# Kernel optimization log

Hardware: AMD Instinct MI355X
Metric: run time of the kernel (lower is better)

## Reference

```python
import jax, jax.numpy as jnp
import numpy as np

N0, N1, N2 = 20000, 15000, 15000
N = N0 + N1 + N2          # total nodes
E = 800000                # edges
H, D = 4, 64              # heads, hidden per head
ED = 64                   # edge feature dim
NET = 8                   # num edge types
C = 16                    # num classes
SLOPE = 0.2               # leaky relu negative slope
ALPHA = 0.05              # residual-attention mixing

def _glorot(key, shape):
    return jax.random.normal(key, shape, dtype=jnp.float32) / jnp.sqrt(jnp.float32(shape[-1]))

def setup_inputs() -> dict:
    key = jax.random.key(0)
    ks = jax.random.split(key, 32)
    return {
        "x0": jax.random.normal(ks[0], (N0, 128), jnp.float32),
        "x1": jax.random.normal(ks[1], (N1, 64), jnp.float32),
        "x2": jax.random.normal(ks[2], (N2, 32), jnp.float32),
        "src": jax.random.randint(ks[3], (E,), 0, N),
        "dst": jax.random.randint(ks[4], (E,), 0, N),
        "efeat": jax.random.randint(ks[5], (E,), 0, NET),
        # per-node-type input projections (fc_list)
        "W0": _glorot(ks[6], (64, 128)), "b0": jnp.zeros((64,), jnp.float32),
        "W1": _glorot(ks[7], (64, 64)),  "b1": jnp.zeros((64,), jnp.float32),
        "W2": _glorot(ks[8], (64, 32)),  "b2": jnp.zeros((64,), jnp.float32),
        # GAT layer 0: in 64 -> H*D, no residual, elu
        "Wg0": _glorot(ks[9], (H * D, 64)),
        "etab0": _glorot(ks[10], (NET, ED)),
        "We0": _glorot(ks[11], (H * ED, ED)),
        "al0": _glorot(ks[12], (H, D)), "ar0": _glorot(ks[13], (H, D)), "ae0": _glorot(ks[14], (H, ED)),
        # GAT layer 1: in H*D -> H*D, identity residual, elu
        "Wg1": _glorot(ks[15], (H * D, H * D)),
        "etab1": _glorot(ks[16], (NET, ED)),
        "We1": _glorot(ks[17], (H * ED, ED)),
        "al1": _glorot(ks[18], (H, D)), "ar1": _glorot(ks[19], (H, D)), "ae1": _glorot(ks[20], (H, ED)),
        # final GAT layer: in H*D -> 1*C, linear residual, no activation
        "Wg2": _glorot(ks[21], (C, H * D)),
        "etab2": _glorot(ks[22], (NET, ED)),
        "We2": _glorot(ks[23], (ED, ED)),
        "al2": _glorot(ks[24], (1, C)), "ar2": _glorot(ks[25], (1, C)), "ae2": _glorot(ks[26], (1, ED)),
        "resW2": _glorot(ks[27], (C, H * D)),
    }

def _edge_softmax(scores, dst):
    # softmax over incoming edges of each dst node; scores: [E, H]
    m = jax.ops.segment_max(scores, dst, num_segments=N)
    ex = jnp.exp(scores - m[dst])
    s = jax.ops.segment_sum(ex, dst, num_segments=N)
    return ex / (s[dst] + 1e-9)

def _gat_conv(h, src, dst, et, Wg, etab, We, al, ar, ae, res_attn, res, resW, act):
    nH, oD = al.shape
    feat = (h @ Wg.T).reshape(N, nH, oD)                 # [N,H,D]
    ee = (etab[et] @ We.T).reshape(E, nH, -1)            # [E,H,ED]
    el = jnp.einsum('nhd,hd->nh', feat, al)
    er = jnp.einsum('nhd,hd->nh', feat, ar)
    es = jnp.einsum('ehd,hd->eh', ee, ae)
    logits = jax.nn.leaky_relu(el[src] + er[dst] + es, SLOPE)
    a = _edge_softmax(logits, dst)                       # [E,H]
    if res_attn is not None:
        a = a * (1.0 - ALPHA) + res_attn * ALPHA
    out = jax.ops.segment_sum(a[:, :, None] * feat[src], dst, num_segments=N)
    if res:
        resval = (h @ resW.T).reshape(N, -1, oD) if resW is not None else h.reshape(N, nH, oD)
        out = out + resval
    if act is not None:
        out = act(out)
    return out, jax.lax.stop_gradient(a)                 # attention detached (res_attn)

def reference(x0, x1, x2, src, dst, efeat, W0, b0, W1, b1, W2, b2,
              Wg0, etab0, We0, al0, ar0, ae0,
              Wg1, etab1, We1, al1, ar1, ae1,
              Wg2, etab2, We2, al2, ar2, ae2, resW2):
    h = jnp.concatenate([x0 @ W0.T + b0, x1 @ W1.T + b1, x2 @ W2.T + b2], axis=0)  # [N,64]
    h, ra = _gat_conv(h, src, dst, efeat, Wg0, etab0, We0, al0, ar0, ae0, None, False, None, jax.nn.elu)
    h = h.reshape(N, -1)
    h, ra = _gat_conv(h, src, dst, efeat, Wg1, etab1, We1, al1, ar1, ae1, ra, True, None, jax.nn.elu)
    h = h.reshape(N, -1)
    logits, _ = _gat_conv(h, src, dst, efeat, Wg2, etab2, We2, al2, ar2, ae2, None, True, resW2, None)
    return logits.mean(axis=1)                           # [N, C]
```

## Files before the change

### kernel.cpp

```cpp
#include <hip/hip_runtime.h>
#include <math.h>

#define N0 20000
#define N1 15000
#define N2 15000
#define NN 50000
#define EE 800000
#define SLOPE 0.2f
#define ALPHA 0.05f

typedef _Float16 h8 __attribute__((ext_vector_type(8)));
typedef _Float16 h4 __attribute__((ext_vector_type(4)));
typedef float f4v __attribute__((ext_vector_type(4)));

__device__ __forceinline__ float sel4(float4 v, int h) {
    float lo = (h & 1) ? v.y : v.x;
    float hi = (h & 1) ? v.w : v.z;
    return (h & 2) ? hi : lo;
}

__device__ __forceinline__ float elu_fast(float x) {
    return x > 0.f ? x : __expf(x) - 1.f;
}


__global__ void hist_kernel(const int* __restrict__ dst, int* __restrict__ deg, int E_) {
    int e = blockIdx.x * blockDim.x + threadIdx.x;
    if (e < E_) atomicAdd(&deg[dst[e]], 1);
}

__global__ __launch_bounds__(256) void block_sum_kernel(const int* __restrict__ deg,
                                                        int* __restrict__ bsum, int n) {
    int i = blockIdx.x * 256 + threadIdx.x;
    int v = (i < n) ? deg[i] : 0;
    #pragma unroll
    for (int off = 32; off > 0; off >>= 1) v += __shfl_down(v, off);
    __shared__ int sh[4];
    if ((threadIdx.x & 63) == 0) sh[threadIdx.x >> 6] = v;
    __syncthreads();
    if (threadIdx.x == 0) bsum[blockIdx.x] = sh[0] + sh[1] + sh[2] + sh[3];
}

__global__ __launch_bounds__(256) void scan_out2(const int* __restrict__ deg,
                                                 const int* __restrict__ bsum,
                                                 int* __restrict__ rowstart,
                                                 int* __restrict__ cursor, int n, int nb) {
    __shared__ int sb[256];
    __shared__ int boff_s;
    int tid = threadIdx.x;
    int v = (tid < nb) ? bsum[tid] : 0;
    sb[tid] = v;
    __syncthreads();
    #pragma unroll
    for (int off = 1; off < 256; off <<= 1) {
        int t = (tid >= off) ? sb[tid - off] : 0;
        __syncthreads();
        sb[tid] += t;
        __syncthreads();
    }
    if (tid == blockIdx.x) boff_s = sb[tid] - v;
    __syncthreads();
    int boff = boff_s;
    int i = blockIdx.x * 256 + tid;
    int d = (i < n) ? deg[i] : 0;
    __syncthreads();
    sb[tid] = d;
    __syncthreads();
    #pragma unroll
    for (int off = 1; off < 256; off <<= 1) {
        int t = (tid >= off) ? sb[tid - off] : 0;
        __syncthreads();
        sb[tid] += t;
        __syncthreads();
    }
    int excl = sb[tid] - d + boff;
    if (i < n) { rowstart[i] = excl; cursor[i] = excl; }
    if (i == n - 1) rowstart[n] = excl + d;
}

__global__ void scatter_kernel(const int* __restrict__ src, const int* __restrict__ dst,
                               const int* __restrict__ et, int* __restrict__ cursor,
                               int* __restrict__ pk, int E_) {
    int e = blockIdx.x * blockDim.x + threadIdx.x;
    if (e >= E_) return;
    int d = dst[e];
    int p = atomicAdd(&cursor[d], 1);
    pk[p] = (et[e] << 16) | src[e];
}


__device__ __forceinline__ void es_pair(int p,
                                        const float* __restrict__ etab0, const float* __restrict__ We0, const float* __restrict__ ae0,
                                        const float* __restrict__ etab1, const float* __restrict__ We1, const float* __restrict__ ae1,
                                        const float* __restrict__ etab2, const float* __restrict__ We2, const float* __restrict__ ae2,
                                        float* __restrict__ es) {
    const float *etab, *We, *ae;
    float* out;
    int H;
    if (p < 32)      { etab = etab0; We = We0; ae = ae0; out = es;      H = 4; }
    else if (p < 64) { p -= 32; etab = etab1; We = We1; ae = ae1; out = es + 32; H = 4; }
    else             { p -= 64; etab = etab2; We = We2; ae = ae2; out = es + 64; H = 1; }
    int t = p / H, h = p % H;
    int j = threadIdx.x & 63;
    const float* w = We + (size_t)(h * 64 + j) * 64;
    const float* e = etab + t * 64;
    float s = 0.f;
    #pragma unroll
    for (int k = 0; k < 64; k += 4) {
        float4 wv = *(const float4*)(w + k);
        float4 ev = *(const float4*)(e + k);
        s += wv.x * ev.x + wv.y * ev.y + wv.z * ev.z + wv.w * ev.w;
    }
    s *= ae[h * 64 + j];
    #pragma unroll
    for (int off = 32; off > 0; off >>= 1) s += __shfl_down(s, off);
    if (j == 0) out[t * H + h] = s;
}

__global__ __launch_bounds__(256) void prep_kernel(
        const float* etab0, const float* We0, const float* ae0,
        const float* etab1, const float* We1, const float* ae1,
        const float* etab2, const float* We2, const float* ae2,
        float* es,
        const float* s0, _Float16* d0, int n0,
        const float* s1, _Float16* d1, int n1,
        const float* s2, _Float16* d2, int n2,
        const float* s3, _Float16* d3, int n3,
        const float* s4, _Float16* d4, int n4,
        const float* s5, _Float16* d5, int n5,
        const float* s6, _Float16* d6, int n6,
        const float* s7, _Float16* d7, int n7,
        const float* s8, _Float16* d8, int n8,
        const float* s9, _Float16* d9, int n9) {
    int b = blockIdx.x;
    if (b < 18) {
        int p = b * 4 + (threadIdx.x >> 6);
        if (p < 72) es_pair(p, etab0, We0, ae0, etab1, We1, ae1, etab2, We2, ae2, es);
        return;
    }
    int t = (b - 18) * 256 + threadIdx.x;
    if (t < n0) { d0[t] = (_Float16)s0[t]; return; } t -= n0;
    if (t < n1) { d1[t] = (_Float16)s1[t]; return; } t -= n1;
    if (t < n2) { d2[t] = (_Float16)s2[t]; return; } t -= n2;
    if (t < n3) { d3[t] = (_Float16)s3[t]; return; } t -= n3;
    if (t < n4) { d4[t] = (_Float16)s4[t]; return; } t -= n4;
    if (t < n5) { d5[t] = (_Float16)s5[t]; return; } t -= n5;
    if (t < n6) { d6[t] = (_Float16)s6[t]; return; } t -= n6;
    if (t < n7) { d7[t] = (_Float16)s7[t]; return; } t -= n7;
    if (t < n8) { d8[t] = (_Float16)s8[t]; return; } t -= n8;
    if (t < n9) { d9[t] = (_Float16)s9[t]; }
}


template<int NT, int ELR>
__device__ __forceinline__ void gemm_body(int bx, int by,
                                          const _Float16* __restrict__ A,
                                          const _Float16* __restrict__ B,
                                          const float* __restrict__ bias,
                                          float* __restrict__ Cf,
                                          _Float16* __restrict__ Ch,
                                          float* __restrict__ el,
                                          float* __restrict__ er,
                                          const float* __restrict__ al,
                                          const float* __restrict__ ar,
                                          int M, int N, int K) {
    const int wave = threadIdx.x >> 6;
    const int lane = threadIdx.x & 63;
    const int m_base = (bx * 4 + wave) * 32;
    const int n_base = by * (NT * 16);
    const int row = lane & 15;
    const int kq = (lane >> 4) * 8;

    f4v acc[2][NT];
    #pragma unroll
    for (int i = 0; i < 2; i++)
        #pragma unroll
        for (int j = 0; j < NT; j++) {
            f4v z = {0.f, 0.f, 0.f, 0.f};
            acc[i][j] = z;
        }

    int ra = m_base + row;       if (ra >= M) ra = M - 1;
    int rb2 = m_base + 16 + row; if (rb2 >= M) rb2 = M - 1;
    const _Float16* a0p = A + (size_t)ra * K + kq;
    const _Float16* a1p = A + (size_t)rb2 * K + kq;
    const _Float16* bp  = B + (size_t)(n_base + row) * K + kq;

    for (int k = 0; k < K; k += 32) {
        h8 a0 = *(const h8*)(a0p + k);
        h8 a1 = *(const h8*)(a1p + k);
        #pragma unroll
        for (int j = 0; j < NT; j++) {
            h8 b = *(const h8*)(bp + (size_t)j * 16 * K + k);
            acc[0][j] = __builtin_amdgcn_mfma_f32_16x16x32_f16(a0, b, acc[0][j], 0, 0, 0);
            acc[1][j] = __builtin_amdgcn_mfma_f32_16x16x32_f16(a1, b, acc[1][j], 0, 0, 0);
        }
    }

    const int col = lane & 15;
    const int rb = (lane >> 4) * 4;

    if (ELR == 1) {
        float alw[NT], arw[NT];
        #pragma unroll
        for (int j = 0; j < NT; j++) {
            int cg = n_base + j * 16 + col;
            int hg = cg >> 6, d = cg & 63;
            alw[j] = al[hg * 64 + d];
            arw[j] = ar[hg * 64 + d];
        }
        const int hb = n_base >> 6;
        #pragma unroll
        for (int ms = 0; ms < 2; ms++) {
            #pragma unroll
            for (int r = 0; r < 4; r++) {
                float e0 = 0.f, e1 = 0.f, f0 = 0.f, f1 = 0.f;
                #pragma unroll
                for (int j = 0; j < NT; j++) {
                    float av = acc[ms][j][r];
                    if (j < NT / 2) { e0 = fmaf(av, alw[j], e0); f0 = fmaf(av, arw[j], f0); }
                    else            { e1 = fmaf(av, alw[j], e1); f1 = fmaf(av, arw[j], f1); }
                }
                #pragma unroll
                for (int off = 1; off <= 8; off <<= 1) {
                    e0 += __shfl_xor(e0, off);
                    e1 += __shfl_xor(e1, off);
                    f0 += __shfl_xor(f0, off);
                    f1 += __shfl_xor(f1, off);
                }
                int m = m_base + ms * 16 + rb + r;
                if (col == 0 && m < M) {
                    el[m * 4 + hb]     = e0;
                    el[m * 4 + hb + 1] = e1;
                    er[m * 4 + hb]     = f0;
                    er[m * 4 + hb + 1] = f1;
                }
            }
        }
    }
    if (ELR == 2) {
        float alw = al[col], arw = ar[col];
        #pragma unroll
        for (int ms = 0; ms < 2; ms++) {
            #pragma unroll
            for (int r = 0; r < 4; r++) {
                float e = acc[ms][0][r] * alw;
                float f = acc[ms][0][r] * arw;
                #pragma unroll
                for (int off = 1; off <= 8; off <<= 1) {
                    e += __shfl_xor(e, off);
                    f += __shfl_xor(f, off);
                }
                int m = m_base + ms * 16 + rb + r;
                if (col == 0 && m < M) { el[m] = e; er[m] = f; }
            }
        }
    }

    #pragma unroll
    for (int ms = 0; ms < 2; ms++) {
        #pragma unroll
        for (int j = 0; j < NT; j++) {
            #pragma unroll
            for (int r = 0; r < 4; r++) {
                int m = m_base + ms * 16 + rb + r;
                if (m < M) {
                    int n = n_base + j * 16 + col;
                    float v = acc[ms][j][r];
                    if (bias) v += bias[n];
                    if (Cf) Cf[(size_t)m * N + n] = v;
                    if (Ch) Ch[(size_t)m * N + n] = (_Float16)v;
                }
            }
        }
    }
}

template<int NT, int ELR>
__global__ __launch_bounds__(256) void gemm_mfma(const _Float16* __restrict__ A,
                                                 const _Float16* __restrict__ B,
                                                 const float* __restrict__ bias,
                                                 float* __restrict__ Cf,
                                                 _Float16* __restrict__ Ch,
                                                 float* __restrict__ el,
                                                 float* __restrict__ er,
                                                 const float* __restrict__ al,
                                                 const float* __restrict__ ar,
                                                 int M, int N, int K) {
    gemm_body<NT, ELR>(blockIdx.x, blockIdx.y, A, B, bias, Cf, Ch, el, er, al, ar, M, N, K);
}

__global__ __launch_bounds__(256) void proj3(const _Float16* __restrict__ x0h, const _Float16* __restrict__ W0h, const float* __restrict__ b0,
                                             const _Float16* __restrict__ x1h, const _Float16* __restrict__ W1h, const float* __restrict__ b1,
                                             const _Float16* __restrict__ x2h, const _Float16* __restrict__ W2h, const float* __restrict__ b2,
                                             _Float16* __restrict__ h0h, int nb0, int nb1) {
    int b = blockIdx.x;
    if (b < nb0) {
        gemm_body<4, 0>(b, 0, x0h, W0h, b0, nullptr, h0h,
                        nullptr, nullptr, nullptr, nullptr, N0, 64, 128);
    } else if (b < nb0 + nb1) {
        gemm_body<4, 0>(b - nb0, 0, x1h, W1h, b1, nullptr, h0h + (size_t)N0 * 64,
                        nullptr, nullptr, nullptr, nullptr, N1, 64, 64);
    } else {
        gemm_body<4, 0>(b - nb0 - nb1, 0, x2h, W2h, b2, nullptr, h0h + (size_t)(N0 + N1) * 64,
                        nullptr, nullptr, nullptr, nullptr, N2, 64, 32);
    }
}


template<bool WRITE_A, bool HAS_PREV, bool HAS_RES>
__global__ __launch_bounds__(256) void gat_fused4(const int* __restrict__ rowstart,
                                                  const int* __restrict__ pk,
                                                  const float* __restrict__ el,
                                                  const float* __restrict__ er,
                                                  const float* __restrict__ es,
                                                  const _Float16* __restrict__ feat,
                                                  const _Float16* __restrict__ aprev,
                                                  _Float16* __restrict__ awrite,
                                                  const _Float16* __restrict__ resh,
                                                  _Float16* __restrict__ outh, int nN) {
    __shared__ int2 as_lds[4][4][66];
    const int wave = threadIdx.x >> 6;
    const int lane = threadIdx.x & 63;
    int n = blockIdx.x * 4 + wave;
    if (n >= nN) return;
    const int r0 = rowstart[n], r1 = rowstart[n + 1];
    const int deg = r1 - r0;
    float4 er4 = *(const float4*)(er + n * 4);

    if (deg <= 64) {
        const int idx = r0 + lane;
        const bool act = idx < r1;
        int p = act ? pk[idx] : 0;
        int psrc = p & 0xFFFF;
        float4 v4 = {-INFINITY, -INFINITY, -INFINITY, -INFINITY};
        if (act) {
            float4 e4 = *(const float4*)(el + psrc * 4);
            float4 c4 = *(const float4*)(es + (p >> 16) * 4);
            float v;
            v = e4.x + er4.x + c4.x; v4.x = v > 0.f ? v : SLOPE * v;
            v = e4.y + er4.y + c4.y; v4.y = v > 0.f ? v : SLOPE * v;
            v = e4.z + er4.z + c4.z; v4.z = v > 0.f ? v : SLOPE * v;
            v = e4.w + er4.w + c4.w; v4.w = v > 0.f ? v : SLOPE * v;
        }
        float4 m4 = v4;
        #pragma unroll
        for (int off = 1; off <= 8; off <<= 1) {
            m4.x = fmaxf(m4.x, __shfl_xor(m4.x, off));
            m4.y = fmaxf(m4.y, __shfl_xor(m4.y, off));
            m4.z = fmaxf(m4.z, __shfl_xor(m4.z, off));
            m4.w = fmaxf(m4.w, __shfl_xor(m4.w, off));
        }
        if (deg > 16) {
            m4.x = fmaxf(m4.x, __shfl_xor(m4.x, 16));
            m4.y = fmaxf(m4.y, __shfl_xor(m4.y, 16));
            m4.z = fmaxf(m4.z, __shfl_xor(m4.z, 16));
            m4.w = fmaxf(m4.w, __shfl_xor(m4.w, 16));
        }
        if (deg > 32) {
            m4.x = fmaxf(m4.x, __shfl_xor(m4.x, 32));
            m4.y = fmaxf(m4.y, __shfl_xor(m4.y, 32));
            m4.z = fmaxf(m4.z, __shfl_xor(m4.z, 32));
            m4.w = fmaxf(m4.w, __shfl_xor(m4.w, 32));
        }
        float4 ex = {0.f, 0.f, 0.f, 0.f};
        if (act) {
            ex.x = __expf(v4.x - m4.x);
            ex.y = __expf(v4.y - m4.y);
            ex.z = __expf(v4.z - m4.z);
            ex.w = __expf(v4.w - m4.w);
        }
        float4 s4 = ex;
        #pragma unroll
        for (int off = 1; off <= 8; off <<= 1) {
            s4.x += __shfl_xor(s4.x, off);
            s4.y += __shfl_xor(s4.y, off);
            s4.z += __shfl_xor(s4.z, off);
            s4.w += __shfl_xor(s4.w, off);
        }
        if (deg > 16) {
            s4.x += __shfl_xor(s4.x, 16);
            s4.y += __shfl_xor(s4.y, 16);
            s4.z += __shfl_xor(s4.z, 16);
            s4.w += __shfl_xor(s4.w, 16);
        }
        if (deg > 32) {
            s4.x += __shfl_xor(s4.x, 32);
            s4.y += __shfl_xor(s4.y, 32);
            s4.z += __shfl_xor(s4.z, 32);
            s4.w += __shfl_xor(s4.w, 32);
        }
        float4 a4;
        a4.x = ex.x / (s4.x + 1e-9f);
        a4.y = ex.y / (s4.y + 1e-9f);
        a4.z = ex.z / (s4.z + 1e-9f);
        a4.w = ex.w / (s4.w + 1e-9f);
        if (HAS_PREV && act) {
            h4 pv = *(const h4*)(aprev + (size_t)idx * 4);
            a4.x = a4.x * (1.f - ALPHA) + ALPHA * (float)pv[0];
            a4.y = a4.y * (1.f - ALPHA) + ALPHA * (float)pv[1];
            a4.z = a4.z * (1.f - ALPHA) + ALPHA * (float)pv[2];
            a4.w = a4.w * (1.f - ALPHA) + ALPHA * (float)pv[3];
        }
        if (WRITE_A && act) {
            h4 aw;
            aw[0] = (_Float16)a4.x; aw[1] = (_Float16)a4.y;
            aw[2] = (_Float16)a4.z; aw[3] = (_Float16)a4.w;
            *(h4*)(awrite + (size_t)idx * 4) = aw;
        }
        as_lds[wave][0][lane] = make_int2(__float_as_int(a4.x), psrc);
        as_lds[wave][1][lane] = make_int2(__float_as_int(a4.y), psrc);
        as_lds[wave][2][lane] = make_int2(__float_as_int(a4.z), psrc);
        as_lds[wave][3][lane] = make_int2(__float_as_int(a4.w), psrc);

        const int half = lane >> 5;
        const int fl = lane & 31;
        const int h = fl >> 3;
        float acc8[8];
        #pragma unroll
        for (int q = 0; q < 8; q++) acc8[q] = 0.f;
        int i = r0;
        for (; i + 7 < r1; i += 8) {
            int j0 = (i - r0) + half;
            int2 e0 = as_lds[wave][h][j0 + 0];
            int2 e1 = as_lds[wave][h][j0 + 2];
            int2 e2 = as_lds[wave][h][j0 + 4];
            int2 e3 = as_lds[wave][h][j0 + 6];
            float a0 = __int_as_float(e0.x), a1 = __int_as_float(e1.x);
            float a2 = __int_as_float(e2.x), a3 = __int_as_float(e3.x);
            h8 f0 = *(const h8*)(feat + (size_t)e0.y * 256 + fl * 8);
            h8 f1 = *(const h8*)(feat + (size_t)e1.y * 256 + fl * 8);
            h8 f2 = *(const h8*)(feat + (size_t)e2.y * 256 + fl * 8);
            h8 f3 = *(const h8*)(feat + (size_t)e3.y * 256 + fl * 8);
            #pragma unroll
            for (int q = 0; q < 8; q++) acc8[q] = fmaf(a0, (float)f0[q], acc8[q]);
            #pragma unroll
            for (int q = 0; q < 8; q++) acc8[q] = fmaf(a1, (float)f1[q], acc8[q]);
            #pragma unroll
            for (int q = 0; q < 8; q++) acc8[q] = fmaf(a2, (float)f2[q], acc8[q]);
            #pragma unroll
            for (int q = 0; q < 8; q++) acc8[q] = fmaf(a3, (float)f3[q], acc8[q]);
        }
        for (; i + 3 < r1; i += 4) {
            int j0 = (i - r0) + half;
            int2 e0 = as_lds[wave][h][j0 + 0];
            int2 e1 = as_lds[wave][h][j0 + 2];
            float a0 = __int_as_float(e0.x), a1 = __int_as_float(e1.x);
            h8 f0 = *(const h8*)(feat + (size_t)e0.y * 256 + fl * 8);
            h8 f1 = *(const h8*)(feat + (size_t)e1.y * 256 + fl * 8);
            #pragma unroll
            for (int q = 0; q < 8; q++) acc8[q] = fmaf(a0, (float)f0[q], acc8[q]);
            #pragma unroll
            for (int q = 0; q < 8; q++) acc8[q] = fmaf(a1, (float)f1[q], acc8[q]);
        }
        for (; i + 1 < r1; i += 2) {
            int j0 = (i - r0) + half;
            int2 e0 = as_lds[wave][h][j0];
            float a0 = __int_as_float(e0.x);
            h8 f0 = *(const h8*)(feat + (size_t)e0.y * 256 + fl * 8);
            #pragma unroll
            for (int q = 0; q < 8; q++) acc8[q] = fmaf(a0, (float)f0[q], acc8[q]);
        }
        if (i < r1) {
            int j0 = i - r0;
            int2 e0 = as_lds[wave][h][j0];
            float a0 = (half == 0) ? __int_as_float(e0.x) : 0.f;
            h8 f0 = *(const h8*)(feat + (size_t)e0.y * 256 + fl * 8);
            #pragma unroll
            for (int q = 0; q < 8; q++) acc8[q] = fmaf(a0, (float)f0[q], acc8[q]);
        }
        #pragma unroll
        for (int q = 0; q < 8; q++) acc8[q] += __shfl_xor(acc8[q], 32);

        if (half == 0) {
            if (HAS_RES) {
                h8 rv = *(const h8*)(resh + (size_t)n * 256 + fl * 8);
                #pragma unroll
                for (int q = 0; q < 8; q++) acc8[q] += (float)rv[q];
            }
            #pragma unroll
            for (int q = 0; q < 8; q++) acc8[q] = elu_fast(acc8[q]);
            h8 o;
            #pragma unroll
            for (int q = 0; q < 8; q++) o[q] = (_Float16)acc8[q];
            *(h8*)(outh + (size_t)n * 256 + fl * 8) = o;
        }
        return;
    }

    float4 m4 = {-INFINITY, -INFINITY, -INFINITY, -INFINITY};
    for (int base = r0; base < r1; base += 64) {
        int idx = base + lane;
        if (idx < r1) {
            int p = pk[idx];
            float4 e4 = *(const float4*)(el + (p & 0xFFFF) * 4);
            float4 c4 = *(const float4*)(es + (p >> 16) * 4);
            float v;
            v = e4.x + er4.x + c4.x; v = v > 0.f ? v : SLOPE * v; m4.x = fmaxf(m4.x, v);
            v = e4.y + er4.y + c4.y; v = v > 0.f ? v : SLOPE * v; m4.y = fmaxf(m4.y, v);
            v = e4.z + er4.z + c4.z; v = v > 0.f ? v : SLOPE * v; m4.z = fmaxf(m4.z, v);
            v = e4.w + er4.w + c4.w; v = v > 0.f ? v : SLOPE * v; m4.w = fmaxf(m4.w, v);
        }
    }
    #pragma unroll
    for (int off = 1; off < 64; off <<= 1) {
        m4.x = fmaxf(m4.x, __shfl_xor(m4.x, off));
        m4.y = fmaxf(m4.y, __shfl_xor(m4.y, off));
        m4.z = fmaxf(m4.z, __shfl_xor(m4.z, off));
        m4.w = fmaxf(m4.w, __shfl_xor(m4.w, off));
    }
    float4 s4 = {0.f, 0.f, 0.f, 0.f};
    for (int base = r0; base < r1; base += 64) {
        int idx = base + lane;
        if (idx < r1) {
            int p = pk[idx];
            float4 e4 = *(const float4*)(el + (p & 0xFFFF) * 4);
            float4 c4 = *(const float4*)(es + (p >> 16) * 4);
            float4 exv;
            float v;
            v = e4.x + er4.x + c4.x; v = v > 0.f ? v : SLOPE * v; exv.x = __expf(v - m4.x);
            v = e4.y + er4.y + c4.y; v = v > 0.f ? v : SLOPE * v; exv.y = __expf(v - m4.y);
            v = e4.z + er4.z + c4.z; v = v > 0.f ? v : SLOPE * v; exv.z = __expf(v - m4.z);
            v = e4.w + er4.w + c4.w; v = v > 0.f ? v : SLOPE * v; exv.w = __expf(v - m4.w);
            if (base == r0) {
                as_lds[wave][0][lane] = make_int2(__float_as_int(exv.x), p & 0xFFFF);
                as_lds[wave][1][lane] = make_int2(__float_as_int(exv.y), p & 0xFFFF);
                as_lds[wave][2][lane] = make_int2(__float_as_int(exv.z), p & 0xFFFF);
                as_lds[wave][3][lane] = make_int2(__float_as_int(exv.w), p & 0xFFFF);
            }
            s4.x += exv.x; s4.y += exv.y; s4.z += exv.z; s4.w += exv.w;
        }
    }
    #pragma unroll
    for (int off = 1; off < 64; off <<= 1) {
        s4.x += __shfl_xor(s4.x, off);
        s4.y += __shfl_xor(s4.y, off);
        s4.z += __shfl_xor(s4.z, off);
        s4.w += __shfl_xor(s4.w, off);
    }
    float4 inv4;
    inv4.x = 1.f / (s4.x + 1e-9f); inv4.y = 1.f / (s4.y + 1e-9f);
    inv4.z = 1.f / (s4.z + 1e-9f); inv4.w = 1.f / (s4.w + 1e-9f);
    {
        int idx = r0 + lane;
        float4 a;
        a.x = __int_as_float(as_lds[wave][0][lane].x) * inv4.x;
        a.y = __int_as_float(as_lds[wave][1][lane].x) * inv4.y;
        a.z = __int_as_float(as_lds[wave][2][lane].x) * inv4.z;
        a.w = __int_as_float(as_lds[wave][3][lane].x) * inv4.w;
        if (HAS_PREV) {
            h4 pv = *(const h4*)(aprev + (size_t)idx * 4);
            a.x = a.x * (1.f - ALPHA) + ALPHA * (float)pv[0];
            a.y = a.y * (1.f - ALPHA) + ALPHA * (float)pv[1];
            a.z = a.z * (1.f - ALPHA) + ALPHA * (float)pv[2];
            a.w = a.w * (1.f - ALPHA) + ALPHA * (float)pv[3];
        }
        if (WRITE_A) {
            h4 aw;
            aw[0] = (_Float16)a.x; aw[1] = (_Float16)a.y;
            aw[2] = (_Float16)a.z; aw[3] = (_Float16)a.w;
            *(h4*)(awrite + (size_t)idx * 4) = aw;
        }
        as_lds[wave][0][lane].x = __float_as_int(a.x);
        as_lds[wave][1][lane].x = __float_as_int(a.y);
        as_lds[wave][2][lane].x = __float_as_int(a.z);
        as_lds[wave][3][lane].x = __float_as_int(a.w);
    }
    if (WRITE_A) {
        for (int base = r0 + 64; base < r1; base += 64) {
            int idx = base + lane;
            if (idx < r1) {
                int p = pk[idx];
                float4 e4 = *(const float4*)(el + (p & 0xFFFF) * 4);
                float4 c4 = *(const float4*)(es + (p >> 16) * 4);
                float4 a;
                float v;
                v = e4.x + er4.x + c4.x; v = v > 0.f ? v : SLOPE * v; a.x = __expf(v - m4.x) * inv4.x;
                v = e4.y + er4.y + c4.y; v = v > 0.f ? v : SLOPE * v; a.y = __expf(v - m4.y) * inv4.y;
                v = e4.z + er4.z + c4.z; v = v > 0.f ? v : SLOPE * v; a.z = __expf(v - m4.z) * inv4.z;
                v = e4.w + er4.w + c4.w; v = v > 0.f ? v : SLOPE * v; a.w = __expf(v - m4.w) * inv4.w;
                if (HAS_PREV) {
                    h4 pv = *(const h4*)(aprev + (size_t)idx * 4);
                    a.x = a.x * (1.f - ALPHA) + ALPHA * (float)pv[0];
                    a.y = a.y * (1.f - ALPHA) + ALPHA * (float)pv[1];
                    a.z = a.z * (1.f - ALPHA) + ALPHA * (float)pv[2];
                    a.w = a.w * (1.f - ALPHA) + ALPHA * (float)pv[3];
                }
                h4 aw;
                aw[0] = (_Float16)a.x; aw[1] = (_Float16)a.y;
                aw[2] = (_Float16)a.z; aw[3] = (_Float16)a.w;
                *(h4*)(awrite + (size_t)idx * 4) = aw;
            }
        }
    }
    const int h = lane >> 4;
    float4 acc = {0.f, 0.f, 0.f, 0.f};
    const int cap = r0 + 64;
    for (int i = r0; i < cap; i++) {
        int2 e0 = as_lds[wave][h][i - r0];
        h4 f = *(const h4*)(feat + (size_t)e0.y * 256 + lane * 4);
        float av = __int_as_float(e0.x);
        acc.x = fmaf(av, (float)f[0], acc.x);
        acc.y = fmaf(av, (float)f[1], acc.y);
        acc.z = fmaf(av, (float)f[2], acc.z);
        acc.w = fmaf(av, (float)f[3], acc.w);
    }
    {
        float mh = sel4(m4, h), invh = sel4(inv4, h), erh = sel4(er4, h);
        for (int i = cap; i < r1; i++) {
            int p = pk[i];
            int s = p & 0xFFFF, t = p >> 16;
            float v = el[s * 4 + h] + erh + es[t * 4 + h];
            v = v > 0.f ? v : SLOPE * v;
            float a = __expf(v - mh) * invh;
            if (HAS_PREV) a = a * (1.f - ALPHA) + ALPHA * (float)aprev[(size_t)i * 4 + h];
            h4 f = *(const h4*)(feat + (size_t)s * 256 + lane * 4);
            acc.x = fmaf(a, (float)f[0], acc.x);
            acc.y = fmaf(a, (float)f[1], acc.y);
            acc.z = fmaf(a, (float)f[2], acc.z);
            acc.w = fmaf(a, (float)f[3], acc.w);
        }
    }
    if (HAS_RES) {
        h4 rv = *(const h4*)(resh + (size_t)n * 256 + lane * 4);
        acc.x += (float)rv[0]; acc.y += (float)rv[1];
        acc.z += (float)rv[2]; acc.w += (float)rv[3];
    }
    acc.x = elu_fast(acc.x);
    acc.y = elu_fast(acc.y);
    acc.z = elu_fast(acc.z);
    acc.w = elu_fast(acc.w);
    h4 o;
    o[0] = (_Float16)acc.x; o[1] = (_Float16)acc.y;
    o[2] = (_Float16)acc.z; o[3] = (_Float16)acc.w;
    *(h4*)(outh + (size_t)n * 256 + lane * 4) = o;
}


__global__ __launch_bounds__(256) void gat_fused1(const int* __restrict__ rowstart,
                                                  const int* __restrict__ pk,
                                                  const float* __restrict__ el,
                                                  const float* __restrict__ er,
                                                  const float* __restrict__ es,
                                                  const _Float16* __restrict__ cpack,
                                                  float* __restrict__ out, int nN) {
    const int wave = threadIdx.x >> 6;
    const int lane = threadIdx.x & 63;
    int n = blockIdx.x * 4 + wave;
    if (n >= nN) return;
    const int r0 = rowstart[n], r1 = rowstart[n + 1];
    const int deg = r1 - r0;
    const float ern = er[n];

    if (deg <= 64) {
        const int idx = r0 + lane;
        const bool act = idx < r1;
        int p = act ? pk[idx] : 0;
        int psrc = p & 0xFFFF;
        float v = -INFINITY;
        if (act) {
            float t = el[psrc] + ern + es[p >> 16];
            v = t > 0.f ? t : SLOPE * t;
        }
        float m = v;
        #pragma unroll
        for (int off = 1; off <= 8; off <<= 1) m = fmaxf(m, __shfl_xor(m, off));
        if (deg > 16) m = fmaxf(m, __shfl_xor(m, 16));
        if (deg > 32) m = fmaxf(m, __shfl_xor(m, 32));
        float ex = act ? __expf(v - m) : 0.f;
        float s = ex;
        #pragma unroll
        for (int off = 1; off <= 8; off <<= 1) s += __shfl_xor(s, off);
        if (deg > 16) s += __shfl_xor(s, 16);
        if (deg > 32) s += __shfl_xor(s, 32);
        float a = ex / (s + 1e-9f);

        const int eslot = lane >> 4, fl = lane & 15;
        float acc = 0.f;
        int i = r0;
        for (; i + 7 < r1; i += 8) {
            int j0 = (i - r0) + eslot;
            int j1 = j0 + 4;
            int s0 = __shfl(psrc, j0);
            int s1 = __shfl(psrc, j1);
            float a0 = __shfl(a, j0);
            float a1 = __shfl(a, j1);
            float f0 = (float)cpack[(size_t)s0 * 32 + fl];
            float f1 = (float)cpack[(size_t)s1 * 32 + fl];
            acc = fmaf(a0, f0, acc);
            acc = fmaf(a1, f1, acc);
        }
        for (; i + 3 < r1; i += 4) {
            int j = (i - r0) + eslot;
            int sj = __shfl(psrc, j);
            float aj = __shfl(a, j);
            acc = fmaf(aj, (float)cpack[(size_t)sj * 32 + fl], acc);
        }
        int rem = r1 - i;
        if (rem > 0) {
            int j = (i - r0) + (eslot < rem ? eslot : rem - 1);
            int sj = __shfl(psrc, j);
            float aj = __shfl(a, j);
            if (eslot >= rem) aj = 0.f;
            acc = fmaf(aj, (float)cpack[(size_t)sj * 32 + fl], acc);
        }
        acc += __shfl_xor(acc, 16);
        acc += __shfl_xor(acc, 32);
        if (lane < 16) out[(size_t)n * 16 + lane] = acc + (float)cpack[(size_t)n * 32 + 16 + lane];
        return;
    }

    float m = -INFINITY;
    for (int base = r0; base < r1; base += 64) {
        int idx = base + lane;
        if (idx < r1) {
            int p = pk[idx];
            float v = el[p & 0xFFFF] + ern + es[p >> 16];
            v = v > 0.f ? v : SLOPE * v;
            m = fmaxf(m, v);
        }
    }
    #pragma unroll
    for (int off = 1; off < 64; off <<= 1) m = fmaxf(m, __shfl_xor(m, off));
    float s = 0.f;
    for (int base = r0; base < r1; base += 64) {
        int idx = base + lane;
        if (idx < r1) {
            int p = pk[idx];
            float v = el[p & 0xFFFF] + ern + es[p >> 16];
            v = v > 0.f ? v : SLOPE * v;
            s += __expf(v - m);
        }
    }
    #pragma unroll
    for (int off = 1; off < 64; off <<= 1) s += __shfl_xor(s, off);
    float inv = 1.f / (s + 1e-9f);
    const int eslot = lane >> 4, fl = lane & 15;
    float acc = 0.f;
    for (int i = r0; i < r1; i += 4) {
        int rem = r1 - i;
        if (eslot < rem) {
            int j = i + eslot;
            int p = pk[j];
            float v = el[p & 0xFFFF] + ern + es[p >> 16];
            v = v > 0.f ? v : SLOPE * v;
            float a = __expf(v - m) * inv;
            acc = fmaf(a, (float)cpack[(size_t)(p & 0xFFFF) * 32 + fl], acc);
        }
    }
    acc += __shfl_xor(acc, 16);
    acc += __shfl_xor(acc, 32);
    if (lane < 16) out[(size_t)n * 16 + lane] = acc + (float)cpack[(size_t)n * 32 + 16 + lane];
}


extern "C" void kernel_launch(void* const* d_in, const int* in_sizes, int n_in,
                              void* d_out, int out_size, void* d_ws, size_t ws_size,
                              hipStream_t stream) {
    const float* x0 = (const float*)d_in[0];
    const float* x1 = (const float*)d_in[1];
    const float* x2 = (const float*)d_in[2];
    const int* src  = (const int*)d_in[3];
    const int* dst  = (const int*)d_in[4];
    const int* et   = (const int*)d_in[5];
    const float* W0 = (const float*)d_in[6];  const float* b0 = (const float*)d_in[7];
    const float* W1 = (const float*)d_in[8];  const float* b1 = (const float*)d_in[9];
    const float* W2 = (const float*)d_in[10]; const float* b2 = (const float*)d_in[11];
    const float* Wg0 = (const float*)d_in[12]; const float* etab0 = (const float*)d_in[13];
    const float* We0 = (const float*)d_in[14]; const float* al0 = (const float*)d_in[15];
    const float* ar0 = (const float*)d_in[16]; const float* ae0 = (const float*)d_in[17];
    const float* Wg1 = (const float*)d_in[18]; const float* etab1 = (const float*)d_in[19];
    const float* We1 = (const float*)d_in[20]; const float* al1 = (const float*)d_in[21];
    const float* ar1 = (const float*)d_in[22]; const float* ae1 = (const float*)d_in[23];
    const float* Wg2 = (const float*)d_in[24]; const float* etab2 = (const float*)d_in[25];
    const float* We2 = (const float*)d_in[26]; const float* al2 = (const float*)d_in[27];
    const float* ar2 = (const float*)d_in[28]; const float* ae2 = (const float*)d_in[29];
    const float* resW2 = (const float*)d_in[30];
    float* outp = (float*)d_out;

    char* p = (char*)d_ws;
    auto alloc = [&](size_t bytes) -> void* {
        void* r = (void*)p;
        p += (bytes + 255) & ~(size_t)255;
        return r;
    };
    _Float16* x0h   = (_Float16*)alloc((size_t)N0 * 128 * 2);
    _Float16* x1h   = (_Float16*)alloc((size_t)N1 * 64 * 2);
    _Float16* x2h   = (_Float16*)alloc((size_t)N2 * 32 * 2);
    _Float16* W0h   = (_Float16*)alloc(64 * 128 * 2);
    _Float16* W1h   = (_Float16*)alloc(64 * 64 * 2);
    _Float16* W2h   = (_Float16*)alloc(64 * 32 * 2);
    _Float16* Wg0h  = (_Float16*)alloc(256 * 64 * 2);
    _Float16* Wg1h  = (_Float16*)alloc(256 * 256 * 2);
    _Float16* wpkh  = (_Float16*)alloc(32 * 256 * 2);
    _Float16* h0h   = (_Float16*)alloc((size_t)NN * 64 * 2);
    _Float16* feath = (_Float16*)alloc((size_t)NN * 256 * 2);
    _Float16* bufAh = (_Float16*)alloc((size_t)NN * 256 * 2);
    _Float16* bufBh = (_Float16*)alloc((size_t)NN * 256 * 2);
    _Float16* a0h   = (_Float16*)alloc((size_t)EE * 4 * 2);
    _Float16* cpackh = (_Float16*)alloc((size_t)NN * 32 * 2);
    float* el    = (float*)alloc((size_t)NN * 4 * 4);
    float* er    = (float*)alloc((size_t)NN * 4 * 4);
    float* es    = (float*)alloc(96 * 4);
    int* rowstart = (int*)alloc((size_t)(NN + 1) * 4);
    int* deg      = (int*)alloc((size_t)NN * 4);
    int* cursor   = (int*)alloc((size_t)NN * 4);
    int* bsum     = (int*)alloc(256 * 4);
    int* pk       = (int*)alloc((size_t)EE * 4);

    const int EB = (EE + 255) / 256;
    const int NB = (NN + 255) / 256;
    const int MB128 = (NN + 127) / 128;
    const int WB = (NN + 3) / 4;
    const int nb0 = (N0 + 127) / 128;
    const int nb1 = (N1 + 127) / 128;
    const int nb2 = (N2 + 127) / 128;

    hipMemsetAsync(deg, 0, (size_t)NN * 4, stream);
    hist_kernel<<<EB, 256, 0, stream>>>(dst, deg, EE);
    block_sum_kernel<<<NB, 256, 0, stream>>>(deg, bsum, NN);
    scan_out2<<<NB, 256, 0, stream>>>(deg, bsum, rowstart, cursor, NN, NB);
    scatter_kernel<<<EB, 256, 0, stream>>>(src, dst, et, cursor, pk, EE);

    {
        int n0c = N0 * 128, n1c = N1 * 64, n2c = N2 * 32;
        int total = n0c + n1c + n2c + 8192 + 4096 + 2048 + 16384 + 65536 + 4096 + 4096;
        prep_kernel<<<18 + (total + 255) / 256, 256, 0, stream>>>(
            etab0, We0, ae0, etab1, We1, ae1, etab2, We2, ae2, es,
            x0, x0h, n0c, x1, x1h, n1c, x2, x2h, n2c,
            W0, W0h, 8192, W1, W1h, 4096, W2, W2h, 2048,
            Wg0, Wg0h, 16384, Wg1, Wg1h, 65536,
            Wg2, wpkh, 4096, resW2, wpkh + 4096, 4096);
    }

    proj3<<<nb0 + nb1 + nb2, 256, 0, stream>>>(x0h, W0h, b0, x1h, W1h, b1, x2h, W2h, b2,
                                               h0h, nb0, nb1);

    gemm_mfma<8, 1><<<dim3(MB128, 2), 256, 0, stream>>>(h0h, Wg0h, nullptr, nullptr, feath,
                                                        el, er, al0, ar0, NN, 256, 64);
    gat_fused4<true, false, false><<<WB, 256, 0, stream>>>(
        rowstart, pk, el, er, es + 0, feath, nullptr, a0h, nullptr, bufAh, NN);

    gemm_mfma<8, 1><<<dim3(MB128, 2), 256, 0, stream>>>(bufAh, Wg1h, nullptr, nullptr, feath,
                                                        el, er, al1, ar1, NN, 256, 256);
    gat_fused4<false, true, true><<<WB, 256, 0, stream>>>(
        rowstart, pk, el, er, es + 32, feath, a0h, nullptr, bufAh, bufBh, NN);

    gemm_mfma<2, 2><<<dim3(MB128, 1), 256, 0, stream>>>(bufBh, wpkh, nullptr, nullptr, cpackh,
                                                        el, er, al2, ar2, NN, 32, 256);
    gat_fused1<<<WB, 256, 0, stream>>>(rowstart, pk, el, er, es + 64, cpackh, outp, NN);
}
```

Baseline: 474.2 us.

## Merge CSR-build stages into prep, projection and first GEMM launches

```diff
diff --git a/kernel.cpp b/kernel.cpp
--- a/kernel.cpp
+++ b/kernel.cpp
@@ -21,71 +21,6 @@
 
 __device__ __forceinline__ float elu_fast(float x) {
     return x > 0.f ? x : __expf(x) - 1.f;
-}
-
-
-__global__ void hist_kernel(const int* __restrict__ dst, int* __restrict__ deg, int E_) {
-    int e = blockIdx.x * blockDim.x + threadIdx.x;
-    if (e < E_) atomicAdd(&deg[dst[e]], 1);
-}
-
-__global__ __launch_bounds__(256) void block_sum_kernel(const int* __restrict__ deg,
-                                                        int* __restrict__ bsum, int n) {
-    int i = blockIdx.x * 256 + threadIdx.x;
-    int v = (i < n) ? deg[i] : 0;
-    #pragma unroll
-    for (int off = 32; off > 0; off >>= 1) v += __shfl_down(v, off);
-    __shared__ int sh[4];
-    if ((threadIdx.x & 63) == 0) sh[threadIdx.x >> 6] = v;
-    __syncthreads();
-    if (threadIdx.x == 0) bsum[blockIdx.x] = sh[0] + sh[1] + sh[2] + sh[3];
-}
-
-__global__ __launch_bounds__(256) void scan_out2(const int* __restrict__ deg,
-                                                 const int* __restrict__ bsum,
-                                                 int* __restrict__ rowstart,
-                                                 int* __restrict__ cursor, int n, int nb) {
-    __shared__ int sb[256];
-    __shared__ int boff_s;
-    int tid = threadIdx.x;
-    int v = (tid < nb) ? bsum[tid] : 0;
-    sb[tid] = v;
-    __syncthreads();
-    #pragma unroll
-    for (int off = 1; off < 256; off <<= 1) {
-        int t = (tid >= off) ? sb[tid - off] : 0;
-        __syncthreads();
-        sb[tid] += t;
-        __syncthreads();
-    }
-    if (tid == blockIdx.x) boff_s = sb[tid] - v;
-    __syncthreads();
-    int boff = boff_s;
-    int i = blockIdx.x * 256 + tid;
-    int d = (i < n) ? deg[i] : 0;
-    __syncthreads();
-    sb[tid] = d;
-    __syncthreads();
-    #pragma unroll
-    for (int off = 1; off < 256; off <<= 1) {
-        int t = (tid >= off) ? sb[tid - off] : 0;
-        __syncthreads();
-        sb[tid] += t;
-        __syncthreads();
-    }
-    int excl = sb[tid] - d + boff;
-    if (i < n) { rowstart[i] = excl; cursor[i] = excl; }
-    if (i == n - 1) rowstart[n] = excl + d;
-}
-
-__global__ void scatter_kernel(const int* __restrict__ src, const int* __restrict__ dst,
-                               const int* __restrict__ et, int* __restrict__ cursor,
-                               int* __restrict__ pk, int E_) {
-    int e = blockIdx.x * blockDim.x + threadIdx.x;
-    if (e >= E_) return;
-    int d = dst[e];
-    int p = atomicAdd(&cursor[d], 1);
-    pk[p] = (et[e] << 16) | src[e];
 }
 
 
@@ -117,7 +52,17 @@
     if (j == 0) out[t * H + h] = s;
 }
 
-__global__ __launch_bounds__(256) void prep_kernel(
+__device__ __forceinline__ void cvt4(const float* __restrict__ s, _Float16* __restrict__ d, int t) {
+    float4 v = ((const float4*)s)[t];
+    h4 o;
+    o[0] = (_Float16)v.x; o[1] = (_Float16)v.y;
+    o[2] = (_Float16)v.z; o[3] = (_Float16)v.w;
+    ((h4*)d)[t] = o;
+}
+
+
+__global__ __launch_bounds__(256) void k1_hist_prep(
+        const int* __restrict__ dst, int* __restrict__ deg,
         const float* etab0, const float* We0, const float* ae0,
         const float* etab1, const float* We1, const float* ae1,
         const float* etab2, const float* We2, const float* ae2,
@@ -131,24 +76,80 @@
         const float* s6, _Float16* d6, int n6,
         const float* s7, _Float16* d7, int n7,
         const float* s8, _Float16* d8, int n8,
-        const float* s9, _Float16* d9, int n9) {
+        const float* s9, _Float16* d9, int n9, int EB) {
     int b = blockIdx.x;
+    if (b < EB) {
+        int e = b * 256 + threadIdx.x;
+        if (e < EE) atomicAdd(&deg[dst[e]], 1);
+        return;
+    }
+    b -= EB;
     if (b < 18) {
         int p = b * 4 + (threadIdx.x >> 6);
         if (p < 72) es_pair(p, etab0, We0, ae0, etab1, We1, ae1, etab2, We2, ae2, es);
         return;
     }
     int t = (b - 18) * 256 + threadIdx.x;
-    if (t < n0) { d0[t] = (_Float16)s0[t]; return; } t -= n0;
-    if (t < n1) { d1[t] = (_Float16)s1[t]; return; } t -= n1;
-    if (t < n2) { d2[t] = (_Float16)s2[t]; return; } t -= n2;
-    if (t < n3) { d3[t] = (_Float16)s3[t]; return; } t -= n3;
-    if (t < n4) { d4[t] = (_Float16)s4[t]; return; } t -= n4;
-    if (t < n5) { d5[t] = (_Float16)s5[t]; return; } t -= n5;
-    if (t < n6) { d6[t] = (_Float16)s6[t]; return; } t -= n6;
-    if (t < n7) { d7[t] = (_Float16)s7[t]; return; } t -= n7;
-    if (t < n8) { d8[t] = (_Float16)s8[t]; return; } t -= n8;
-    if (t < n9) { d9[t] = (_Float16)s9[t]; }
+    if (t < (n0 >> 2)) { cvt4(s0, d0, t); return; } t -= n0 >> 2;
+    if (t < (n1 >> 2)) { cvt4(s1, d1, t); return; } t -= n1 >> 2;
+    if (t < (n2 >> 2)) { cvt4(s2, d2, t); return; } t -= n2 >> 2;
+    if (t < (n3 >> 2)) { cvt4(s3, d3, t); return; } t -= n3 >> 2;
+    if (t < (n4 >> 2)) { cvt4(s4, d4, t); return; } t -= n4 >> 2;
+    if (t < (n5 >> 2)) { cvt4(s5, d5, t); return; } t -= n5 >> 2;
+    if (t < (n6 >> 2)) { cvt4(s6, d6, t); return; } t -= n6 >> 2;
+    if (t < (n7 >> 2)) { cvt4(s7, d7, t); return; } t -= n7 >> 2;
+    if (t < (n8 >> 2)) { cvt4(s8, d8, t); return; } t -= n8 >> 2;
+    if (t < (n9 >> 2)) { cvt4(s9, d9, t); }
+}
+
+
+__device__ __forceinline__ void block_sum_body(int b, const int* __restrict__ deg,
+                                               int* __restrict__ bsum, int n) {
+    int i = b * 256 + threadIdx.x;
+    int v = (i < n) ? deg[i] : 0;
+    #pragma unroll
+    for (int off = 32; off > 0; off >>= 1) v += __shfl_down(v, off);
+    __shared__ int sh[4];
+    if ((threadIdx.x & 63) == 0) sh[threadIdx.x >> 6] = v;
+    __syncthreads();
+    if (threadIdx.x == 0) bsum[b] = sh[0] + sh[1] + sh[2] + sh[3];
+}
+
+__global__ __launch_bounds__(256) void scan_out2(const int* __restrict__ deg,
+                                                 const int* __restrict__ bsum,
+                                                 int* __restrict__ rowstart,
+                                                 int* __restrict__ cursor, int n, int nb) {
+    __shared__ int sb[256];
+    __shared__ int boff_s;
+    int tid = threadIdx.x;
+    int v = (tid < nb) ? bsum[tid] : 0;
+    sb[tid] = v;
+    __syncthreads();
+    #pragma unroll
+    for (int off = 1; off < 256; off <<= 1) {
+        int t = (tid >= off) ? sb[tid - off] : 0;
+        __syncthreads();
+        sb[tid] += t;
+        __syncthreads();
+    }
+    if (tid == blockIdx.x) boff_s = sb[tid] - v;
+    __syncthreads();
+    int boff = boff_s;
+    int i = blockIdx.x * 256 + tid;
+    int d = (i < n) ? deg[i] : 0;
+    __syncthreads();
+    sb[tid] = d;
+    __syncthreads();
+    #pragma unroll
+    for (int off = 1; off < 256; off <<= 1) {
+        int t = (tid >= off) ? sb[tid - off] : 0;
+        __syncthreads();
+        sb[tid] += t;
+        __syncthreads();
+    }
+    int excl = sb[tid] - d + boff;
+    if (i < n) { rowstart[i] = excl; cursor[i] = excl; }
+    if (i == n - 1) rowstart[n] = excl + d;
 }
 
 
@@ -290,11 +291,16 @@
     gemm_body<NT, ELR>(blockIdx.x, blockIdx.y, A, B, bias, Cf, Ch, el, er, al, ar, M, N, K);
 }
 
-__global__ __launch_bounds__(256) void proj3(const _Float16* __restrict__ x0h, const _Float16* __restrict__ W0h, const float* __restrict__ b0,
-                                             const _Float16* __restrict__ x1h, const _Float16* __restrict__ W1h, const float* __restrict__ b1,
-                                             const _Float16* __restrict__ x2h, const _Float16* __restrict__ W2h, const float* __restrict__ b2,
-                                             _Float16* __restrict__ h0h, int nb0, int nb1) {
+
+__global__ __launch_bounds__(256) void k2_bsum_proj(
+        const int* __restrict__ deg, int* __restrict__ bsum, int NBv,
+        const _Float16* __restrict__ x0h, const _Float16* __restrict__ W0h, const float* __restrict__ b0,
+        const _Float16* __restrict__ x1h, const _Float16* __restrict__ W1h, const float* __restrict__ b1,
+        const _Float16* __restrict__ x2h, const _Float16* __restrict__ W2h, const float* __restrict__ b2,
+        _Float16* __restrict__ h0h, int nb0, int nb1) {
     int b = blockIdx.x;
+    if (b < NBv) { block_sum_body(b, deg, bsum, NN); return; }
+    b -= NBv;
     if (b < nb0) {
         gemm_body<4, 0>(b, 0, x0h, W0h, b0, nullptr, h0h,
                         nullptr, nullptr, nullptr, nullptr, N0, 64, 128);
@@ -305,6 +311,28 @@
         gemm_body<4, 0>(b - nb0 - nb1, 0, x2h, W2h, b2, nullptr, h0h + (size_t)(N0 + N1) * 64,
                         nullptr, nullptr, nullptr, nullptr, N2, 64, 32);
     }
+}
+
+
+__global__ __launch_bounds__(256) void k4_scat_gemm0(
+        const int* __restrict__ src, const int* __restrict__ dst, const int* __restrict__ et,
+        int* __restrict__ cursor, int* __restrict__ pk, int EB,
+        const _Float16* __restrict__ h0h, const _Float16* __restrict__ Wg0h,
+        _Float16* __restrict__ feath, float* __restrict__ el, float* __restrict__ er,
+        const float* __restrict__ al0, const float* __restrict__ ar0, int MB) {
+    int b = blockIdx.x;
+    if (b < EB) {
+        int e = b * 256 + threadIdx.x;
+        if (e < EE) {
+            int d = dst[e];
+            int p = atomicAdd(&cursor[d], 1);
+            pk[p] = (et[e] << 16) | src[e];
+        }
+        return;
+    }
+    int t = b - EB;
+    int bx = t % MB, by = t / MB;
+    gemm_body<8, 1>(bx, by, h0h, Wg0h, nullptr, nullptr, feath, el, er, al0, ar0, NN, 256, 64);
 }
 
 
@@ -817,27 +845,29 @@
     const int nb2 = (N2 + 127) / 128;
 
     hipMemsetAsync(deg, 0, (size_t)NN * 4, stream);
-    hist_kernel<<<EB, 256, 0, stream>>>(dst, deg, EE);
-    block_sum_kernel<<<NB, 256, 0, stream>>>(deg, bsum, NN);
-    scan_out2<<<NB, 256, 0, stream>>>(deg, bsum, rowstart, cursor, NN, NB);
-    scatter_kernel<<<EB, 256, 0, stream>>>(src, dst, et, cursor, pk, EE);
 
     {
         int n0c = N0 * 128, n1c = N1 * 64, n2c = N2 * 32;
-        int total = n0c + n1c + n2c + 8192 + 4096 + 2048 + 16384 + 65536 + 4096 + 4096;
-        prep_kernel<<<18 + (total + 255) / 256, 256, 0, stream>>>(
+        int total4 = (n0c + n1c + n2c + 8192 + 4096 + 2048 + 16384 + 65536 + 4096 + 4096) / 4;
+        int cvb = (total4 + 255) / 256;
+        k1_hist_prep<<<EB + 18 + cvb, 256, 0, stream>>>(
+            dst, deg,
             etab0, We0, ae0, etab1, We1, ae1, etab2, We2, ae2, es,
             x0, x0h, n0c, x1, x1h, n1c, x2, x2h, n2c,
             W0, W0h, 8192, W1, W1h, 4096, W2, W2h, 2048,
             Wg0, Wg0h, 16384, Wg1, Wg1h, 65536,
-            Wg2, wpkh, 4096, resW2, wpkh + 4096, 4096);
-    }
-
-    proj3<<<nb0 + nb1 + nb2, 256, 0, stream>>>(x0h, W0h, b0, x1h, W1h, b1, x2h, W2h, b2,
-                                               h0h, nb0, nb1);
-
-    gemm_mfma<8, 1><<<dim3(MB128, 2), 256, 0, stream>>>(h0h, Wg0h, nullptr, nullptr, feath,
-                                                        el, er, al0, ar0, NN, 256, 64);
+            Wg2, wpkh, 4096, resW2, wpkh + 4096, 4096, EB);
+    }
+
+    k2_bsum_proj<<<NB + nb0 + nb1 + nb2, 256, 0, stream>>>(
+        deg, bsum, NB, x0h, W0h, b0, x1h, W1h, b1, x2h, W2h, b2, h0h, nb0, nb1);
+
+    scan_out2<<<NB, 256, 0, stream>>>(deg, bsum, rowstart, cursor, NN, NB);
+
+    k4_scat_gemm0<<<EB + MB128 * 2, 256, 0, stream>>>(
+        src, dst, et, cursor, pk, EB,
+        h0h, Wg0h, feath, el, er, al0, ar0, MB128);
+
     gat_fused4<true, false, false><<<WB, 256, 0, stream>>>(
         rowstart, pk, el, er, es + 0, feath, nullptr, a0h, nullptr, bufAh, NN);
 
```

After: 464.6 us. -2.0%, faster.
